# Optimization experiments

Hardware: AMD Instinct MI355X
Metric: run time of the kernel (lower is better)

The kernel has to match this reference:

```python
import jax, jax.numpy as jnp
import numpy as np

B = 1048576  # number of particles


def setup_inputs() -> dict:
    key = jax.random.key(0)
    kF, = jax.random.split(key, 1)
    # near-identity deformation gradients: positive det, distinct singular values
    F = jnp.eye(3, dtype=jnp.float32) + 0.1 * jax.random.normal(kF, (B, 3, 3), dtype=jnp.float32)
    return {
        "F": F,
        "youngs_modulus_log": jnp.asarray(11.5, dtype=jnp.float32),
        "poissons_ratio": jnp.asarray(0.3, dtype=jnp.float32),
        "yield_stress": jnp.asarray(1000.0, dtype=jnp.float32),
        "alpha": jnp.asarray(0.3, dtype=jnp.float32),
        "cohesion": jnp.asarray(0.0, dtype=jnp.float32),
    }


def _recompose(U, sigma, Vh):
    # U @ diag(sigma) @ Vh without materializing diag matrices
    return jnp.einsum('bij,bj,bjk->bik', U, sigma, Vh)


def reference(F, youngs_modulus_log, poissons_ratio, yield_stress, alpha, cohesion):
    E = jnp.exp(youngs_modulus_log)
    nu = poissons_ratio
    mu = E / (2.0 * (1.0 + nu))
    la = E * nu / ((1.0 + nu) * (1.0 - 2.0 * nu))

    # single batched 3x3 SVD shared by plasticine and sand branches
    U, s, Vh = jnp.linalg.svd(F)  # (B,3,3), (B,3), (B,3,3)

    # ---- plasticine (von Mises return mapping) ----
    s_p = jnp.maximum(s, 0.01)
    eps = jnp.log(s_p)                              # (B,3)
    tr = jnp.sum(eps, axis=1, keepdims=True)
    eps_bar = eps - tr / 3.0
    eps_bar_norm = jnp.linalg.norm(eps_bar, axis=1, keepdims=True) + 1e-5
    delta_gamma = eps_bar_norm - yield_stress / (2.0 * mu)
    yield_eps = eps - delta_gamma / eps_bar_norm * eps_bar
    sigma_plast = jnp.where(delta_gamma > 0, jnp.exp(yield_eps), s_p)
    F_plasticine = _recompose(U, sigma_plast, Vh)

    # ---- sand (Drucker-Prager return mapping) ----
    s_s = jnp.maximum(s, 0.05)
    eps_s = jnp.log(s_s)
    tr_s = jnp.sum(eps_s, axis=1, keepdims=True)
    eps_hat = eps_s - tr_s / 3.0
    eps_hat_norm = jnp.linalg.norm(eps_hat, axis=1, keepdims=True)
    expand_eps = jnp.full_like(eps_s, 1.0) * cohesion
    shifted_trace = tr_s - cohesion * 3.0
    cond_yield = shifted_trace < 0
    dg = eps_hat_norm + (3.0 * la + 2.0 * mu) / (2.0 * mu) * shifted_trace * alpha
    compress_eps = eps_s - jnp.maximum(dg, 0.0) / eps_hat_norm * eps_hat
    eps_final = jnp.where(cond_yield, compress_eps, expand_eps)
    F_sand = _recompose(U, jnp.exp(eps_final), Vh)

    # ---- water (volume-preserving projection) ----
    J = jnp.linalg.det(F)                            # (B,)
    Je_1_3 = jnp.power(J, 1.0 / 3.0)[:, None]        # (B,1)
    F_water = Je_1_3[:, :, None] * jnp.eye(3, dtype=F.dtype)  # diag(Je^{1/3}) per batch

    return 0.5 * F_plasticine + 0.3 * F_sand + 0.2 * F_water
```

## Files before the change

### kernel.cpp

```cpp
#include <hip/hip_runtime.h>
#include <hip/hip_bf16.h>

#define FRCP(x)  __builtin_amdgcn_rcpf(x)
#define FSQRT(x) __builtin_amdgcn_sqrtf(x)
#define FRSQ(x)  __builtin_amdgcn_rsqf(x)
#define FLOG2(x) __builtin_amdgcn_logf(x)
#define FEXP2(x) __builtin_amdgcn_exp2f(x)

__global__ __launch_bounds__(256) void physics_svd_kernel(
    const float* __restrict__ gF,
    const float* __restrict__ p_Elog,
    const float* __restrict__ p_nu,
    const float* __restrict__ p_ys,
    const float* __restrict__ p_alpha,
    const float* __restrict__ p_coh,
    float* __restrict__ gOut,
    int B)
{
    __shared__ __align__(16) float lds[2304];

    const int tid   = threadIdx.x;
    const int pbase = blockIdx.x * 256;
    const int nhere = min(256, B - pbase);
    const int nflt  = nhere * 9;

    if (nhere == 256) {
        const float4* g4 = reinterpret_cast<const float4*>(gF + (size_t)pbase * 9);
        float4* l4 = reinterpret_cast<float4*>(lds);
        l4[tid]       = g4[tid];
        l4[tid + 256] = g4[tid + 256];
        if (tid < 64) l4[tid + 512] = g4[tid + 512];
    } else {
        for (int j = tid; j < nflt; j += 256) lds[j] = gF[(size_t)pbase * 9 + j];
    }
    __syncthreads();

    const float E  = __expf(p_Elog[0]);
    const float nu = p_nu[0];
    const float ys = p_ys[0];
    const float al = p_alpha[0];
    const float co = p_coh[0];
    const float mu = E / (2.0f * (1.0f + nu));
    const float la = E * nu / ((1.0f + nu) * (1.0f - 2.0f * nu));
    const float ys_2mu = ys / (2.0f * mu);
    const float kk     = (3.0f * la + 2.0f * mu) / (2.0f * mu) * al;
    const float lco2   = co * 1.4426950f;

    const float LN2      = 0.69314718f;
    const float L2_1EM4  = -13.287712f;
    const float L2_25EM4 = -8.6438562f;

    if (tid < nhere) {
        float f[9];
        #pragma unroll
        for (int k = 0; k < 9; ++k) f[k] = lds[tid * 9 + k];

        float b00 = f[0]*f[0] + f[3]*f[3] + f[6]*f[6];
        float b01 = f[0]*f[1] + f[3]*f[4] + f[6]*f[7];
        float b02 = f[0]*f[2] + f[3]*f[5] + f[6]*f[8];
        float b11 = f[1]*f[1] + f[4]*f[4] + f[7]*f[7];
        float b12 = f[1]*f[2] + f[4]*f[5] + f[7]*f[8];
        float b22 = f[2]*f[2] + f[5]*f[5] + f[8]*f[8];

        float a00 = b00, a01 = b01, a02 = b02;
        float a11 = b11, a12 = b12, a22 = b22;

        #define JROT(APP, AQQ, APQ, RP, RQ)                                           \
        {                                                                             \
            float apq = APQ;                                                          \
            float d   = AQQ - APP;                                                    \
            float p2  = apq + apq;                                                    \
            float h   = FSQRT(__builtin_fmaf(d, d, p2 * p2));                         \
            float w_  = FRCP(fabsf(d) + h);                                           \
            float t   = p2 * copysignf(w_, d);                                        \
            t = (apq == 0.0f) ? 0.0f : t;              \
            float c = FRSQ(__builtin_fmaf(t, t, 1.0f));                               \
            float s = t * c;                                                          \
            APP -= t * apq;  AQQ += t * apq;  APQ = 0.0f;                             \
            float pk = RP, qk = RQ;                                                   \
            RP = c*pk - s*qk;  RQ = s*pk + c*qk;                                      \
        }

        #pragma unroll
        for (int sweep = 0; sweep < 3; ++sweep) {
            JROT(a00, a11, a01, a02, a12)
            JROT(a00, a22, a02, a01, a12)
            JROT(a11, a22, a12, a01, a02)
        }
        #undef JROT

        float l0 = fmaxf(a00, 1e-20f);
        float l1 = fmaxf(a11, 1e-20f);
        float l2 = fmaxf(a22, 1e-20f);
        float li0 = FLOG2(l0), li1 = FLOG2(l1), li2 = FLOG2(l2);

        float p0 = 0.5f * fmaxf(li0, L2_1EM4);
        float p1 = 0.5f * fmaxf(li1, L2_1EM4);
        float p2 = 0.5f * fmaxf(li2, L2_1EM4);
        float mp = (p0 + p1 + p2) * (1.0f/3.0f);
        float bb0 = p0 - mp, bb1 = p1 - mp, bb2 = p2 - mp;
        float bn = LN2 * FSQRT(bb0*bb0 + bb1*bb1 + bb2*bb2) + 1e-5f;
        float rp = fmaxf(bn - ys_2mu, 0.0f) * FRCP(bn);

        float q0 = 0.5f * fmaxf(li0, L2_25EM4);
        float q1 = 0.5f * fmaxf(li1, L2_25EM4);
        float q2 = 0.5f * fmaxf(li2, L2_25EM4);
        float mq = (q0 + q1 + q2) * (1.0f/3.0f);
        float hb0 = q0 - mq, hb1 = q1 - mq, hb2 = q2 - mq;
        float hn = LN2 * FSQRT(hb0*hb0 + hb1*hb1 + hb2*hb2);
        float st = LN2 * (q0 + q1 + q2) - 3.0f * co;
        bool cond = st < 0.0f;
        float rs = fmaxf(hn + kk * st, 0.0f) * FRCP(fmaxf(hn, 1e-20f));

        float hl0 = 0.5f * li0, hl1 = 0.5f * li1, hl2 = 0.5f * li2;
        float w0 = 0.5f * FEXP2(p0 - rp*bb0 - hl0)
                 + 0.3f * FEXP2(cond ? (q0 - rs*hb0 - hl0) : (lco2 - hl0));
        float w1 = 0.5f * FEXP2(p1 - rp*bb1 - hl1)
                 + 0.3f * FEXP2(cond ? (q1 - rs*hb1 - hl1) : (lco2 - hl1));
        float w2 = 0.5f * FEXP2(p2 - rp*bb2 - hl2)
                 + 0.3f * FEXP2(cond ? (q2 - rs*hb2 - hl2) : (lco2 - hl2));

        float d10 = l1 - l0, d21 = l2 - l1, d20 = l2 - l0;
        float i10 = FRCP(copysignf(fmaxf(fabsf(d10), 1e-6f), d10));
        float i21 = FRCP(copysignf(fmaxf(fabsf(d21), 1e-6f), d21));
        float i20 = FRCP(copysignf(fmaxf(fabsf(d20), 1e-6f), d20));
        float c1  = (w1 - w0) * i10;
        float w12 = (w2 - w1) * i21;
        float c2  = (w12 - c1) * i20;
        float beta  = c1 - c2 * (l0 + l1);
        float alpha = w0 - c1 * l0 + c2 * l0 * l1;

        float s00 = b00*b00 + b01*b01 + b02*b02;
        float s01 = b00*b01 + b01*b11 + b02*b12;
        float s02 = b00*b02 + b01*b12 + b02*b22;
        float s11 = b01*b01 + b11*b11 + b12*b12;
        float s12 = b01*b02 + b11*b12 + b12*b22;
        float s22 = b02*b02 + b12*b12 + b22*b22;

        float W00 = c2*s00 + beta*b00 + alpha;
        float W01 = c2*s01 + beta*b01;
        float W02 = c2*s02 + beta*b02;
        float W11 = c2*s11 + beta*b11 + alpha;
        float W12 = c2*s12 + beta*b12;
        float W22 = c2*s22 + beta*b22 + alpha;

        float J = f[0]*(f[4]*f[8] - f[5]*f[7])
                - f[1]*(f[3]*f[8] - f[5]*f[6])
                + f[2]*(f[3]*f[7] - f[4]*f[6]);
        float wd = 0.2f * FEXP2(FLOG2(J) * (1.0f/3.0f));

        float o[9];
        o[0] = f[0]*W00 + f[1]*W01 + f[2]*W02 + wd;
        o[1] = f[0]*W01 + f[1]*W11 + f[2]*W12;
        o[2] = f[0]*W02 + f[1]*W12 + f[2]*W22;
        o[3] = f[3]*W00 + f[4]*W01 + f[5]*W02;
        o[4] = f[3]*W01 + f[4]*W11 + f[5]*W12 + wd;
        o[5] = f[3]*W02 + f[4]*W12 + f[5]*W22;
        o[6] = f[6]*W00 + f[7]*W01 + f[8]*W02;
        o[7] = f[6]*W01 + f[7]*W11 + f[8]*W12;
        o[8] = f[6]*W02 + f[7]*W12 + f[8]*W22 + wd;

        #pragma unroll
        for (int k = 0; k < 9; ++k) lds[tid * 9 + k] = o[k];
    }
    __syncthreads();

    if (nhere == 256) {
        float4* g4 = reinterpret_cast<float4*>(gOut + (size_t)pbase * 9);
        const float4* l4 = reinterpret_cast<const float4*>(lds);
        g4[tid]       = l4[tid];
        g4[tid + 256] = l4[tid + 256];
        if (tid < 64) g4[tid + 512] = l4[tid + 512];
    } else {
        for (int j = tid; j < nflt; j += 256)
            gOut[(size_t)pbase * 9 + j] = lds[j];
    }
}

extern "C" void kernel_launch(void* const* d_in, const int* in_sizes, int n_in,
                              void* d_out, int out_size, void* d_ws, size_t ws_size,
                              hipStream_t stream) {
    const float* F      = (const float*)d_in[0];
    const float* p_Elog = (const float*)d_in[1];
    const float* p_nu   = (const float*)d_in[2];
    const float* p_ys   = (const float*)d_in[3];
    const float* p_al   = (const float*)d_in[4];
    const float* p_co   = (const float*)d_in[5];
    float* out = (float*)d_out;

    const int B = in_sizes[0] / 9;
    const int nblocks = (B + 255) / 256;
    physics_svd_kernel<<<nblocks, 256, 0, stream>>>(
        F, p_Elog, p_nu, p_ys, p_al, p_co, out, B);
}
```

Baseline: 102.1 us.

## Replace Jacobi eigen-sweeps with closed-form trigonometric 3x3 eigenvalue solver

Swaps the three-sweep Jacobi diagonalisation of F^T F for a closed-form eigenvalue solution. It builds a cubic-root cos estimate from a polynomial and refines it with one Newton step, cutting the many sqrt/rcp/rsq transcendental ops. It also merges the three divided-difference reciprocals into one reciprocal of their product, and simplifies the log clamps by applying them after halving. The risk is accuracy loss for near-degenerate eigenvalues, and possible overflow or underflow in the product reciprocal.

Result: faster. 99.43 us (-2.6%).

```diff
diff --git a/kernel.cpp b/kernel.cpp
--- a/kernel.cpp
+++ b/kernel.cpp
@@ -3,7 +3,6 @@
 
 #define FRCP(x)  __builtin_amdgcn_rcpf(x)
 #define FSQRT(x) __builtin_amdgcn_sqrtf(x)
-#define FRSQ(x)  __builtin_amdgcn_rsqf(x)
 #define FLOG2(x) __builtin_amdgcn_logf(x)
 #define FEXP2(x) __builtin_amdgcn_exp2f(x)
 
@@ -46,9 +45,9 @@
     const float kk     = (3.0f * la + 2.0f * mu) / (2.0f * mu) * al;
     const float lco2   = co * 1.4426950f;
 
-    const float LN2      = 0.69314718f;
-    const float L2_1EM4  = -13.287712f;
-    const float L2_25EM4 = -8.6438562f;
+    const float LN2     = 0.69314718f;
+    const float L2_001  = -6.6438562f;
+    const float L2_005  = -4.3219281f;
 
     if (tid < nhere) {
         float f[9];
@@ -62,49 +61,47 @@
         float b12 = f[1]*f[2] + f[4]*f[5] + f[7]*f[8];
         float b22 = f[2]*f[2] + f[5]*f[5] + f[8]*f[8];
 
-        float a00 = b00, a01 = b01, a02 = b02;
-        float a11 = b11, a12 = b12, a22 = b22;
+        float m3  = (b00 + b11 + b22) * (1.0f/3.0f);
+        float k00 = b00 - m3, k11 = b11 - m3, k22 = b22 - m3;
+        float pp  = (k00*k00 + k11*k11 + k22*k22) * (1.0f/6.0f)
+                  + (b01*b01 + b02*b02 + b12*b12) * (1.0f/3.0f);
+        float qq  = 0.5f * (k00*(k11*k22 - b12*b12)
+                          - b01*(b01*k22 - b12*b02)
+                          + b02*(b01*b12 - k11*b02));
+        float sp  = FSQRT(pp);
+        float rr  = qq * FRCP(fmaxf(pp * sp, 1e-30f));
+        rr = fminf(fmaxf(rr, -1.0f), 1.0f);
+        float uu = FSQRT(__builtin_fmaf(0.5f, rr, 0.5f));
+        float cc = 0.5f + uu * (0.57735027f + uu * (-0.09914500f + uu * 0.02179470f));
+        float c2v = cc * cc;
+        float fv  = cc * __builtin_fmaf(4.0f, c2v, -3.0f) - rr;
+        float fpv = __builtin_fmaf(12.0f, c2v, -3.0f);
+        cc -= fv * FRCP(fmaxf(fpv, 1e-4f));
+        cc = fminf(fmaxf(cc, 0.5f), 1.0f);
+        float ssin = FSQRT(fmaxf(__builtin_fmaf(-cc, cc, 1.0f), 0.0f));
+        float sp2 = sp + sp;
+        float l0 = __builtin_fmaf(sp2, cc, m3);
+        float ca = __builtin_fmaf(-0.8660254f, ssin, -0.5f * cc);
+        float l1 = __builtin_fmaf(sp2, ca, m3);
+        float l2 = 3.0f * m3 - l0 - l1;
+        l0 = fmaxf(l0, 1e-20f);
+        l1 = fmaxf(l1, 1e-20f);
+        l2 = fmaxf(l2, 1e-20f);
 
-        #define JROT(APP, AQQ, APQ, RP, RQ)                                           \
-        {                                                                             \
-            float apq = APQ;                                                          \
-            float d   = AQQ - APP;                                                    \
-            float p2  = apq + apq;                                                    \
-            float h   = FSQRT(__builtin_fmaf(d, d, p2 * p2));                         \
-            float w_  = FRCP(fabsf(d) + h);                                           \
-            float t   = p2 * copysignf(w_, d);                                        \
-            t = (apq == 0.0f) ? 0.0f : t;              \
-            float c = FRSQ(__builtin_fmaf(t, t, 1.0f));                               \
-            float s = t * c;                                                          \
-            APP -= t * apq;  AQQ += t * apq;  APQ = 0.0f;                             \
-            float pk = RP, qk = RQ;                                                   \
-            RP = c*pk - s*qk;  RQ = s*pk + c*qk;                                      \
-        }
+        float li0 = FLOG2(l0), li1 = FLOG2(l1), li2 = FLOG2(l2);
+        float hl0 = 0.5f * li0, hl1 = 0.5f * li1, hl2 = 0.5f * li2;
 
-        #pragma unroll
-        for (int sweep = 0; sweep < 3; ++sweep) {
-            JROT(a00, a11, a01, a02, a12)
-            JROT(a00, a22, a02, a01, a12)
-            JROT(a11, a22, a12, a01, a02)
-        }
-        #undef JROT
-
-        float l0 = fmaxf(a00, 1e-20f);
-        float l1 = fmaxf(a11, 1e-20f);
-        float l2 = fmaxf(a22, 1e-20f);
-        float li0 = FLOG2(l0), li1 = FLOG2(l1), li2 = FLOG2(l2);
-
-        float p0 = 0.5f * fmaxf(li0, L2_1EM4);
-        float p1 = 0.5f * fmaxf(li1, L2_1EM4);
-        float p2 = 0.5f * fmaxf(li2, L2_1EM4);
+        float p0 = fmaxf(hl0, L2_001);
+        float p1 = fmaxf(hl1, L2_001);
+        float p2 = fmaxf(hl2, L2_001);
         float mp = (p0 + p1 + p2) * (1.0f/3.0f);
         float bb0 = p0 - mp, bb1 = p1 - mp, bb2 = p2 - mp;
         float bn = LN2 * FSQRT(bb0*bb0 + bb1*bb1 + bb2*bb2) + 1e-5f;
         float rp = fmaxf(bn - ys_2mu, 0.0f) * FRCP(bn);
 
-        float q0 = 0.5f * fmaxf(li0, L2_25EM4);
-        float q1 = 0.5f * fmaxf(li1, L2_25EM4);
-        float q2 = 0.5f * fmaxf(li2, L2_25EM4);
+        float q0 = fmaxf(hl0, L2_005);
+        float q1 = fmaxf(hl1, L2_005);
+        float q2 = fmaxf(hl2, L2_005);
         float mq = (q0 + q1 + q2) * (1.0f/3.0f);
         float hb0 = q0 - mq, hb1 = q1 - mq, hb2 = q2 - mq;
         float hn = LN2 * FSQRT(hb0*hb0 + hb1*hb1 + hb2*hb2);
@@ -112,7 +109,6 @@
         bool cond = st < 0.0f;
         float rs = fmaxf(hn + kk * st, 0.0f) * FRCP(fmaxf(hn, 1e-20f));
 
-        float hl0 = 0.5f * li0, hl1 = 0.5f * li1, hl2 = 0.5f * li2;
         float w0 = 0.5f * FEXP2(p0 - rp*bb0 - hl0)
                  + 0.3f * FEXP2(cond ? (q0 - rs*hb0 - hl0) : (lco2 - hl0));
         float w1 = 0.5f * FEXP2(p1 - rp*bb1 - hl1)
@@ -121,9 +117,13 @@
                  + 0.3f * FEXP2(cond ? (q2 - rs*hb2 - hl2) : (lco2 - hl2));
 
         float d10 = l1 - l0, d21 = l2 - l1, d20 = l2 - l0;
-        float i10 = FRCP(copysignf(fmaxf(fabsf(d10), 1e-6f), d10));
-        float i21 = FRCP(copysignf(fmaxf(fabsf(d21), 1e-6f), d21));
-        float i20 = FRCP(copysignf(fmaxf(fabsf(d20), 1e-6f), d20));
+        d10 = copysignf(fmaxf(fabsf(d10), 1e-6f), d10);
+        d21 = copysignf(fmaxf(fabsf(d21), 1e-6f), d21);
+        d20 = copysignf(fmaxf(fabsf(d20), 1e-6f), d20);
+        float invP = FRCP(d10 * d21 * d20);
+        float i10 = d21 * d20 * invP;
+        float i21 = d10 * d20 * invP;
+        float i20 = d10 * d21 * invP;
         float c1  = (w1 - w0) * i10;
         float w12 = (w2 - w1) * i21;
         float c2  = (w12 - c1) * i20;
```
